# Optimization experiments

Hardware: AMD Instinct MI355X
Metric: run time of the kernel (lower is better)

Reference implementation:

```python
import jax, jax.numpy as jnp
import numpy as np

N = 100000   # nodes
E = 640000   # edges
D = 128      # in_channels
C = 40       # out_channels (classes)


def setup_inputs() -> dict:
    key = jax.random.key(0)
    ks = jax.random.split(key, 6)
    x = jax.random.normal(ks[0], (N, D), jnp.float32)
    edge_index = jax.random.randint(ks[1], (2, E), 0, N)
    edge_weight = jax.random.uniform(ks[2], (E,), jnp.float32)
    # 8 block convs (4 blocks x 2) stacked, + final conv
    Wb = jax.random.normal(ks[3], (8, D, D), jnp.float32) / np.sqrt(D)
    bb = jnp.zeros((8, D), jnp.float32)
    Wf = jax.random.normal(ks[4], (D, C), jnp.float32) / np.sqrt(D)
    bf = jnp.zeros((C,), jnp.float32)
    return dict(x=x, edge_index=edge_index, edge_weight=edge_weight,
                Wb=Wb, bb=bb, Wf=Wf, bf=bf)


def _gcn(x, W, b, src, dst, w):
    """PyG GCNConv (normalize=True) with self-loops already appended to src/dst/w."""
    n = x.shape[0]
    h = x @ W                                   # [N, out]
    deg = jax.ops.segment_sum(w, dst, num_segments=n)
    dinv = jnp.where(deg > 0, jax.lax.rsqrt(deg), 0.0)
    norm = dinv[src] * w * dinv[dst]            # [E+N]
    out = jax.ops.segment_sum(h[src] * norm[:, None], dst, num_segments=n)
    return out + b


def reference(x, edge_index, edge_weight, Wb, bb, Wf, bf):
    n = x.shape[0]
    loop = jnp.arange(n)
    src = jnp.concatenate([edge_index[0], loop])
    dst = jnp.concatenate([edge_index[1], loop])
    w = jnp.concatenate([edge_weight, jnp.ones((n,), x.dtype)])
    # forward only runs blocks 1-4 (blocks 5-7 unused in the original forward)
    for i in range(4):
        identity = x
        x = jax.nn.relu(_gcn(x, Wb[2 * i], bb[2 * i], src, dst, w))
        # dropout: identity in eval mode
        x = jax.nn.relu(_gcn(x, Wb[2 * i + 1], bb[2 * i + 1], src, dst, w))
        # F.normalize: row-wise L2 with eps=1e-12
        x = x / jnp.maximum(jnp.linalg.norm(x, axis=1, keepdims=True), 1e-12)
        x = (x + identity) / 2
    x = _gcn(x, Wf, bf, src, dst, w)
    return jax.nn.log_softmax(x, axis=1)
```

## Files before the change

### kernel.cpp

```cpp
#include <hip/hip_runtime.h>
#include <math.h>

#define NN 100000
#define EE 640000
#define DD 128
#define CC 40

typedef __bf16 bf16x8 __attribute__((ext_vector_type(8)));
typedef float f32x4 __attribute__((ext_vector_type(4)));
typedef unsigned short us8 __attribute__((ext_vector_type(8)));

__device__ inline unsigned short f2b(float f) {
    union { float f; unsigned u; } v; v.f = f;
    unsigned u = v.u;
    return (unsigned short)((u + 0x7FFFu + ((u >> 16) & 1u)) >> 16);
}
__device__ inline float b2f(unsigned short b) {
    union { unsigned u; float f; } v; v.u = ((unsigned)b) << 16;
    return v.f;
}


__global__ __launch_bounds__(256) void k_deg_cnt(const int* __restrict__ dst,
                                                 const float* __restrict__ w,
                                                 float* __restrict__ deg,
                                                 int* __restrict__ cnt) {
    int e = blockIdx.x * 256 + threadIdx.x;
    if (e < EE) {
        int d = dst[e];
        atomicAdd(&deg[d], w[e]);
        atomicAdd(&cnt[d], 1);
    }
}

__global__ __launch_bounds__(256) void k_dinv(float* __restrict__ deg) {
    int i = blockIdx.x * 256 + threadIdx.x;
    if (i < NN) deg[i] = rsqrtf(deg[i] + 1.0f);
}

__global__ __launch_bounds__(256) void k_scan1(const int* __restrict__ cnt,
                                               int* __restrict__ out,
                                               int* __restrict__ partial) {
    __shared__ int lds[256];
    int t = threadIdx.x;
    int base = blockIdx.x * 1024 + t * 4;
    int v[4]; int s = 0;
    #pragma unroll
    for (int j = 0; j < 4; ++j) {
        int idx = base + j;
        v[j] = (idx < NN) ? cnt[idx] : 0;
        s += v[j];
    }
    lds[t] = s;
    __syncthreads();
    for (int off = 1; off < 256; off <<= 1) {
        int x = lds[t];
        int y = (t >= off) ? lds[t - off] : 0;
        __syncthreads();
        lds[t] = x + y;
        __syncthreads();
    }
    int excl = lds[t] - s;
    if (t == 255) partial[blockIdx.x] = lds[255];
    int run = excl;
    #pragma unroll
    for (int j = 0; j < 4; ++j) {
        int idx = base + j;
        if (idx < NN) out[idx] = run;
        run += v[j];
    }
}

__global__ __launch_bounds__(128) void k_scan2(int* __restrict__ partial) {
    __shared__ int lds[128];
    int t = threadIdx.x;
    int v = (t < 98) ? partial[t] : 0;
    lds[t] = v;
    __syncthreads();
    for (int off = 1; off < 128; off <<= 1) {
        int x = lds[t];
        int y = (t >= off) ? lds[t - off] : 0;
        __syncthreads();
        lds[t] = x + y;
        __syncthreads();
    }
    if (t < 98) partial[t] = lds[t] - v;
}

__global__ __launch_bounds__(256) void k_scan3(int* __restrict__ rp,
                                               const int* __restrict__ partial) {
    int i = blockIdx.x * 256 + threadIdx.x;
    if (i < NN) rp[i] += partial[i >> 10];
    if (i == 0) rp[NN] = EE;
}

__global__ __launch_bounds__(256) void k_scatter(const int* __restrict__ src,
                                                 const int* __restrict__ dst,
                                                 const float* __restrict__ w,
                                                 const float* __restrict__ dinv,
                                                 const int* __restrict__ rp,
                                                 int* __restrict__ fill,
                                                 int* __restrict__ col,
                                                 float* __restrict__ val) {
    int e = blockIdx.x * 256 + threadIdx.x;
    if (e < EE) {
        int s = src[e], d = dst[e];
        int p = rp[d] + atomicAdd(&fill[d], 1);
        col[p] = s;
        val[p] = dinv[s] * w[e] * dinv[d];
    }
}


__global__ __launch_bounds__(256) void k_prep_w(const float* __restrict__ Wb,
                                                unsigned short* __restrict__ WT) {
    int idx = blockIdx.x * 256 + threadIdx.x;
    if (idx >= 8 * DD * DD) return;
    int m = idx >> 14;
    int n = (idx >> 7) & 127;
    int k = idx & 127;
    WT[idx] = f2b(Wb[(size_t)m * DD * DD + (size_t)k * DD + n]);
}

__global__ __launch_bounds__(256) void k_prep_wf(const float* __restrict__ Wf,
                                                 unsigned short* __restrict__ WfT) {
    int idx = blockIdx.x * 256 + threadIdx.x;
    if (idx >= 48 * DD) return;
    int n = idx >> 7;
    int k = idx & 127;
    WfT[idx] = (n < CC) ? f2b(Wf[(size_t)k * CC + n]) : 0;
}

__global__ __launch_bounds__(256) void k_x2bf(const float* __restrict__ x,
                                              float* __restrict__ A,
                                              unsigned short* __restrict__ Abf) {
    int idx = blockIdx.x * 256 + threadIdx.x;
    if (idx >= NN * DD / 4) return;
    float4 v = ((const float4*)x)[idx];
    ((float4*)A)[idx] = v;
    ushort4 r;
    r.x = f2b(v.x); r.y = f2b(v.y); r.z = f2b(v.z); r.w = f2b(v.w);
    ((ushort4*)Abf)[idx] = r;
}

__global__ __launch_bounds__(256) void k_mm_mfma(const unsigned short* __restrict__ X,
                                                 const unsigned short* __restrict__ WT,
                                                 unsigned short* __restrict__ H) {
    int wid = threadIdx.x >> 6;
    int lane = threadIdx.x & 63;
    int r0 = blockIdx.x * 64 + wid * 16;
    int sl = lane & 15, g = lane >> 4;
    int arow = r0 + sl;
    if (arow >= NN) arow = NN - 1;

    f32x4 acc[8];
    #pragma unroll
    for (int n = 0; n < 8; ++n) acc[n] = (f32x4){0.f, 0.f, 0.f, 0.f};

    const bf16x8* xrow = (const bf16x8*)(X + (size_t)arow * DD);
    #pragma unroll
    for (int kc = 0; kc < 4; ++kc) {
        bf16x8 a = xrow[kc * 4 + g];
        #pragma unroll
        for (int n = 0; n < 8; ++n) {
            const bf16x8* wrow = (const bf16x8*)(WT + (size_t)(n * 16 + sl) * DD);
            bf16x8 b = wrow[kc * 4 + g];
            acc[n] = __builtin_amdgcn_mfma_f32_16x16x32_bf16(a, b, acc[n], 0, 0, 0);
        }
    }
    #pragma unroll
    for (int n = 0; n < 8; ++n) {
        #pragma unroll
        for (int v = 0; v < 4; ++v) {
            int row = r0 + g * 4 + v;
            if (row < NN) H[(size_t)row * DD + n * 16 + sl] = f2b(acc[n][v]);
        }
    }
}

__global__ __launch_bounds__(256) void k_mm_final(const unsigned short* __restrict__ X,
                                                  const unsigned short* __restrict__ WfT,
                                                  const float* __restrict__ bf_,
                                                  float* __restrict__ C40) {
    int wid = threadIdx.x >> 6;
    int lane = threadIdx.x & 63;
    int r0 = blockIdx.x * 64 + wid * 16;
    int sl = lane & 15, g = lane >> 4;
    int arow = r0 + sl;
    if (arow >= NN) arow = NN - 1;

    f32x4 acc[3];
    #pragma unroll
    for (int n = 0; n < 3; ++n) acc[n] = (f32x4){0.f, 0.f, 0.f, 0.f};

    const bf16x8* xrow = (const bf16x8*)(X + (size_t)arow * DD);
    #pragma unroll
    for (int kc = 0; kc < 4; ++kc) {
        bf16x8 a = xrow[kc * 4 + g];
        #pragma unroll
        for (int n = 0; n < 3; ++n) {
            const bf16x8* wrow = (const bf16x8*)(WfT + (size_t)(n * 16 + sl) * DD);
            bf16x8 b = wrow[kc * 4 + g];
            acc[n] = __builtin_amdgcn_mfma_f32_16x16x32_bf16(a, b, acc[n], 0, 0, 0);
        }
    }
    #pragma unroll
    for (int n = 0; n < 3; ++n) {
        int c = n * 16 + sl;
        #pragma unroll
        for (int v = 0; v < 4; ++v) {
            int row = r0 + g * 4 + v;
            if (row < NN && c < CC) C40[(size_t)row * CC + c] = acc[n][v] + bf_[c];
        }
    }
}


#define AGG_CORE(h_, node_, sl_, a_)                                        \
    {                                                                       \
        float dv = dinv[node_];                                             \
        float dv2 = dv * dv;                                                \
        us8 m_ = ((const us8*)(h_ + (size_t)node_ * DD))[sl_];              \
        _Pragma("unroll")                                                   \
        for (int j = 0; j < 8; ++j) a_[j] = dv2 * b2f(m_[j]);               \
        int e = rp[node_], end = rp[node_ + 1];                             \
        for (; e + 2 <= end; e += 2) {                                      \
            int s0 = col[e], s1 = col[e + 1];                               \
            float v0 = val[e], v1 = val[e + 1];                             \
            us8 q0 = ((const us8*)(h_ + (size_t)s0 * DD))[sl_];             \
            us8 q1 = ((const us8*)(h_ + (size_t)s1 * DD))[sl_];             \
            _Pragma("unroll")                                               \
            for (int j = 0; j < 8; ++j) a_[j] += v0 * b2f(q0[j]) + v1 * b2f(q1[j]); \
        }                                                                   \
        if (e < end) {                                                      \
            int s0 = col[e];                                                \
            float v0 = val[e];                                              \
            us8 q0 = ((const us8*)(h_ + (size_t)s0 * DD))[sl_];             \
            _Pragma("unroll")                                               \
            for (int j = 0; j < 8; ++j) a_[j] += v0 * b2f(q0[j]);           \
        }                                                                   \
    }

__global__ __launch_bounds__(256) void k_agg128(const unsigned short* __restrict__ h,
                                                const float* __restrict__ dinv,
                                                const int* __restrict__ rp,
                                                const int* __restrict__ col,
                                                const float* __restrict__ val,
                                                const float* __restrict__ bias,
                                                unsigned short* __restrict__ outb) {
    int node = blockIdx.x * 16 + (threadIdx.x >> 4);
    int sl = threadIdx.x & 15;
    if (node >= NN) return;
    float a[8];
    AGG_CORE(h, node, sl, a);
    float4 bz0 = ((const float4*)bias)[sl * 2];
    float4 bz1 = ((const float4*)bias)[sl * 2 + 1];
    float bb[8] = {bz0.x, bz0.y, bz0.z, bz0.w, bz1.x, bz1.y, bz1.z, bz1.w};
    us8 r;
    #pragma unroll
    for (int j = 0; j < 8; ++j) r[j] = f2b(fmaxf(a[j] + bb[j], 0.f));
    ((us8*)(outb + (size_t)node * DD))[sl] = r;
}

__global__ __launch_bounds__(256) void k_agg128_nr(const unsigned short* __restrict__ h,
                                                   const float* __restrict__ dinv,
                                                   const int* __restrict__ rp,
                                                   const int* __restrict__ col,
                                                   const float* __restrict__ val,
                                                   const float* __restrict__ bias,
                                                   float* __restrict__ A,
                                                   unsigned short* __restrict__ Abf) {
    int node = blockIdx.x * 16 + (threadIdx.x >> 4);
    int sl = threadIdx.x & 15;
    if (node >= NN) return;
    float a[8];
    AGG_CORE(h, node, sl, a);
    float4 bz0 = ((const float4*)bias)[sl * 2];
    float4 bz1 = ((const float4*)bias)[sl * 2 + 1];
    float bb[8] = {bz0.x, bz0.y, bz0.z, bz0.w, bz1.x, bz1.y, bz1.z, bz1.w};
    float ss = 0.f;
    #pragma unroll
    for (int j = 0; j < 8; ++j) {
        a[j] = fmaxf(a[j] + bb[j], 0.f);
        ss += a[j] * a[j];
    }
    ss += __shfl_xor(ss, 1);
    ss += __shfl_xor(ss, 2);
    ss += __shfl_xor(ss, 4);
    ss += __shfl_xor(ss, 8);
    float sc = 1.0f / fmaxf(sqrtf(ss), 1e-12f);
    float4 a0 = ((const float4*)(A + (size_t)node * DD))[sl * 2];
    float4 a1 = ((const float4*)(A + (size_t)node * DD))[sl * 2 + 1];
    float av[8] = {a0.x, a0.y, a0.z, a0.w, a1.x, a1.y, a1.z, a1.w};
    us8 rb;
    #pragma unroll
    for (int j = 0; j < 8; ++j) {
        av[j] = (a[j] * sc + av[j]) * 0.5f;
        rb[j] = f2b(av[j]);
    }
    float4 o0 = {av[0], av[1], av[2], av[3]};
    float4 o1 = {av[4], av[5], av[6], av[7]};
    ((float4*)(A + (size_t)node * DD))[sl * 2] = o0;
    ((float4*)(A + (size_t)node * DD))[sl * 2 + 1] = o1;
    ((us8*)(Abf + (size_t)node * DD))[sl] = rb;
}

__global__ __launch_bounds__(256) void k_agg_plain(const unsigned short* __restrict__ h,
                                                   const float* __restrict__ dinv,
                                                   const int* __restrict__ rp,
                                                   const int* __restrict__ col,
                                                   const float* __restrict__ val,
                                                   unsigned short* __restrict__ outb) {
    int node = blockIdx.x * 16 + (threadIdx.x >> 4);
    int sl = threadIdx.x & 15;
    if (node >= NN) return;
    float a[8];
    AGG_CORE(h, node, sl, a);
    us8 r;
    #pragma unroll
    for (int j = 0; j < 8; ++j) r[j] = f2b(a[j]);
    ((us8*)(outb + (size_t)node * DD))[sl] = r;
}

__global__ __launch_bounds__(256) void k_logsm(const float* __restrict__ Cb,
                                               float* __restrict__ out) {
    int node = blockIdx.x * 4 + (threadIdx.x >> 6);
    int lane = threadIdx.x & 63;
    if (node >= NN) return;
    float v = (lane < CC) ? Cb[(size_t)node * CC + lane] : -3.0e38f;
    float m = v;
    #pragma unroll
    for (int off = 32; off > 0; off >>= 1) m = fmaxf(m, __shfl_xor(m, off));
    float e = (lane < CC) ? expf(v - m) : 0.f;
    float s = e;
    #pragma unroll
    for (int off = 32; off > 0; off >>= 1) s += __shfl_xor(s, off);
    if (lane < CC) out[(size_t)node * CC + lane] = v - m - logf(s);
}


extern "C" void kernel_launch(void* const* d_in, const int* in_sizes, int n_in,
                              void* d_out, int out_size, void* d_ws, size_t ws_size,
                              hipStream_t stream) {
    const float* x  = (const float*)d_in[0];
    const int*   ei = (const int*)d_in[1];
    const float* ew = (const float*)d_in[2];
    const float* Wb = (const float*)d_in[3];
    const float* bb = (const float*)d_in[4];
    const float* Wf = (const float*)d_in[5];
    const float* bf_ = (const float*)d_in[6];
    const int* src = ei;
    const int* dst = ei + EE;
    float* out = (float*)d_out;

    char* p = (char*)d_ws;
    float*          A    = (float*)p;          p += (size_t)NN * DD * 4;
    unsigned short* Abf  = (unsigned short*)p; p += (size_t)NN * DD * 2;
    unsigned short* Bbf  = (unsigned short*)p; p += (size_t)NN * DD * 2;
    unsigned short* Cbf  = (unsigned short*)p; p += (size_t)NN * DD * 2;
    unsigned short* Gbf  = (unsigned short*)p; p += (size_t)NN * DD * 2;
    float*          C40  = (float*)p;          p += (size_t)NN * CC * 4;
    unsigned short* WT   = (unsigned short*)p; p += (size_t)8 * DD * DD * 2;
    unsigned short* WfT  = (unsigned short*)p; p += (size_t)48 * DD * 2;
    float* dinv = (float*)p; p += (size_t)NN * 4;
    int*   cnt  = (int*)p;   p += (size_t)NN * 4;
    int*   rp   = (int*)p;   p += (size_t)(NN + 1) * 4;
    int*   fill = (int*)p;   p += (size_t)NN * 4;
    int*   col  = (int*)p;   p += (size_t)EE * 4;
    float* val  = (float*)p; p += (size_t)EE * 4;
    int*   partial = (int*)p; p += 128 * 4;

    hipMemsetAsync(dinv, 0, (size_t)NN * 4, stream);
    hipMemsetAsync(cnt,  0, (size_t)NN * 4, stream);
    hipMemsetAsync(fill, 0, (size_t)NN * 4, stream);

    k_deg_cnt<<<(EE + 255) / 256, 256, 0, stream>>>(dst, ew, dinv, cnt);
    k_dinv<<<(NN + 255) / 256, 256, 0, stream>>>(dinv);
    k_scan1<<<98, 256, 0, stream>>>(cnt, rp, partial);
    k_scan2<<<1, 128, 0, stream>>>(partial);
    k_scan3<<<(NN + 255) / 256, 256, 0, stream>>>(rp, partial);
    k_scatter<<<(EE + 255) / 256, 256, 0, stream>>>(src, dst, ew, dinv, rp, fill, col, val);

    k_prep_w<<<(8 * DD * DD + 255) / 256, 256, 0, stream>>>(Wb, WT);
    k_prep_wf<<<(48 * DD + 255) / 256, 256, 0, stream>>>(Wf, WfT);
    k_x2bf<<<(NN * DD / 4 + 255) / 256, 256, 0, stream>>>(x, A, Abf);

    for (int blk = 0; blk < 4; ++blk) {
        k_mm_mfma<<<(NN + 63) / 64, 256, 0, stream>>>(Abf, WT + (size_t)(2 * blk) * DD * DD, Bbf);
        k_agg128<<<(NN + 15) / 16, 256, 0, stream>>>(Bbf, dinv, rp, col, val, bb + (size_t)(2 * blk) * DD, Cbf);
        k_mm_mfma<<<(NN + 63) / 64, 256, 0, stream>>>(Cbf, WT + (size_t)(2 * blk + 1) * DD * DD, Bbf);
        k_agg128_nr<<<(NN + 15) / 16, 256, 0, stream>>>(Bbf, dinv, rp, col, val, bb + (size_t)(2 * blk + 1) * DD, A, Abf);
    }
    k_agg_plain<<<(NN + 15) / 16, 256, 0, stream>>>(Abf, dinv, rp, col, val, Gbf);
    k_mm_final<<<(NN + 63) / 64, 256, 0, stream>>>(Gbf, WfT, bf_, C40);
    k_logsm<<<(NN + 3) / 4, 256, 0, stream>>>(C40, out);
}
```

Before: 793.4 us.

## Pack degree and count atomics, fuse log-softmax into final matmul, unroll aggregation

Packs the fixed-point edge-weight degree and the edge count into a single 64-bit atomic. The returned old count is kept as each edge's slot, which removes the separate fill atomics, the dinv kernel and two memsets. Log-softmax is fused into the final MFMA matmul epilogue, so the C40 intermediate round trip and a kernel launch disappear. The CSR aggregation loop is unrolled from 2 to 4 edges per iteration for more memory-level parallelism. Fixed-point degree accumulation adds a small quantization error in the normalization.

```diff
diff --git a/kernel.cpp b/kernel.cpp
--- a/kernel.cpp
+++ b/kernel.cpp
@@ -5,6 +5,7 @@
 #define EE 640000
 #define DD 128
 #define CC 40
+#define FIXS 4194304.0f
 
 typedef __bf16 bf16x8 __attribute__((ext_vector_type(8)));
 typedef float f32x4 __attribute__((ext_vector_type(4)));
@@ -21,24 +22,22 @@
 }
 
 
-__global__ __launch_bounds__(256) void k_deg_cnt(const int* __restrict__ dst,
-                                                 const float* __restrict__ w,
-                                                 float* __restrict__ deg,
-                                                 int* __restrict__ cnt) {
+__global__ __launch_bounds__(256) void k_edge1(const int* __restrict__ dst,
+                                               const float* __restrict__ w,
+                                               unsigned long long* __restrict__ degcnt,
+                                               int* __restrict__ pos) {
     int e = blockIdx.x * 256 + threadIdx.x;
     if (e < EE) {
         int d = dst[e];
-        atomicAdd(&deg[d], w[e]);
-        atomicAdd(&cnt[d], 1);
-    }
-}
-
-__global__ __launch_bounds__(256) void k_dinv(float* __restrict__ deg) {
-    int i = blockIdx.x * 256 + threadIdx.x;
-    if (i < NN) deg[i] = rsqrtf(deg[i] + 1.0f);
-}
-
-__global__ __launch_bounds__(256) void k_scan1(const int* __restrict__ cnt,
+        unsigned long long pk =
+            ((unsigned long long)(unsigned)(w[e] * FIXS) << 32) | 1ull;
+        unsigned long long old = atomicAdd(&degcnt[d], pk);
+        pos[e] = (int)(old & 0xffffffffull);
+    }
+}
+
+__global__ __launch_bounds__(256) void k_scan1(const unsigned long long* __restrict__ degcnt,
+                                               float* __restrict__ dinv,
                                                int* __restrict__ out,
                                                int* __restrict__ partial) {
     __shared__ int lds[256];
@@ -48,8 +47,11 @@
     #pragma unroll
     for (int j = 0; j < 4; ++j) {
         int idx = base + j;
-        v[j] = (idx < NN) ? cnt[idx] : 0;
+        unsigned long long dc = (idx < NN) ? degcnt[idx] : 0ull;
+        v[j] = (int)(dc & 0xffffffffull);
         s += v[j];
+        if (idx < NN)
+            dinv[idx] = rsqrtf((float)(unsigned)(dc >> 32) * (1.0f / FIXS) + 1.0f);
     }
     lds[t] = s;
     __syncthreads();
@@ -99,13 +101,13 @@
                                                  const float* __restrict__ w,
                                                  const float* __restrict__ dinv,
                                                  const int* __restrict__ rp,
-                                                 int* __restrict__ fill,
+                                                 const int* __restrict__ pos,
                                                  int* __restrict__ col,
                                                  float* __restrict__ val) {
     int e = blockIdx.x * 256 + threadIdx.x;
     if (e < EE) {
         int s = src[e], d = dst[e];
-        int p = rp[d] + atomicAdd(&fill[d], 1);
+        int p = rp[d] + pos[e];
         col[p] = s;
         val[p] = dinv[s] * w[e] * dinv[d];
     }
@@ -181,7 +183,7 @@
 __global__ __launch_bounds__(256) void k_mm_final(const unsigned short* __restrict__ X,
                                                   const unsigned short* __restrict__ WfT,
                                                   const float* __restrict__ bf_,
-                                                  float* __restrict__ C40) {
+                                                  float* __restrict__ out) {
     int wid = threadIdx.x >> 6;
     int lane = threadIdx.x & 63;
     int r0 = blockIdx.x * 64 + wid * 16;
@@ -205,12 +207,32 @@
         }
     }
     #pragma unroll
-    for (int n = 0; n < 3; ++n) {
-        int c = n * 16 + sl;
-        #pragma unroll
-        for (int v = 0; v < 4; ++v) {
-            int row = r0 + g * 4 + v;
-            if (row < NN && c < CC) C40[(size_t)row * CC + c] = acc[n][v] + bf_[c];
+    for (int v = 0; v < 4; ++v) {
+        int row = r0 + g * 4 + v;
+        float vv[3];
+        #pragma unroll
+        for (int n = 0; n < 3; ++n) {
+            int c = n * 16 + sl;
+            vv[n] = (c < CC) ? acc[n][v] + bf_[c] : -3.0e38f;
+        }
+        float m = fmaxf(fmaxf(vv[0], vv[1]), vv[2]);
+        m = fmaxf(m, __shfl_xor(m, 1));
+        m = fmaxf(m, __shfl_xor(m, 2));
+        m = fmaxf(m, __shfl_xor(m, 4));
+        m = fmaxf(m, __shfl_xor(m, 8));
+        float s = 0.f;
+        #pragma unroll
+        for (int n = 0; n < 3; ++n)
+            s += (n * 16 + sl < CC) ? expf(vv[n] - m) : 0.f;
+        s += __shfl_xor(s, 1);
+        s += __shfl_xor(s, 2);
+        s += __shfl_xor(s, 4);
+        s += __shfl_xor(s, 8);
+        float ls = logf(s);
+        #pragma unroll
+        for (int n = 0; n < 3; ++n) {
+            int c = n * 16 + sl;
+            if (row < NN && c < CC) out[(size_t)row * CC + c] = vv[n] - m - ls;
         }
     }
 }
@@ -224,15 +246,19 @@
         _Pragma("unroll")                                                   \
         for (int j = 0; j < 8; ++j) a_[j] = dv2 * b2f(m_[j]);               \
         int e = rp[node_], end = rp[node_ + 1];                             \
-        for (; e + 2 <= end; e += 2) {                                      \
-            int s0 = col[e], s1 = col[e + 1];                               \
-            float v0 = val[e], v1 = val[e + 1];                             \
+        for (; e + 4 <= end; e += 4) {                                      \
+            int s0 = col[e], s1 = col[e + 1], s2 = col[e + 2], s3 = col[e + 3]; \
+            float v0 = val[e], v1 = val[e + 1], v2 = val[e + 2], v3 = val[e + 3]; \
             us8 q0 = ((const us8*)(h_ + (size_t)s0 * DD))[sl_];             \
             us8 q1 = ((const us8*)(h_ + (size_t)s1 * DD))[sl_];             \
+            us8 q2 = ((const us8*)(h_ + (size_t)s2 * DD))[sl_];             \
+            us8 q3 = ((const us8*)(h_ + (size_t)s3 * DD))[sl_];             \
             _Pragma("unroll")                                               \
-            for (int j = 0; j < 8; ++j) a_[j] += v0 * b2f(q0[j]) + v1 * b2f(q1[j]); \
+            for (int j = 0; j < 8; ++j)                                     \
+                a_[j] += (v0 * b2f(q0[j]) + v1 * b2f(q1[j]))                \
+                       + (v2 * b2f(q2[j]) + v3 * b2f(q3[j]));               \
         }                                                                   \
-        if (e < end) {                                                      \
+        for (; e < end; ++e) {                                              \
             int s0 = col[e];                                                \
             float v0 = val[e];                                              \
             us8 q0 = ((const us8*)(h_ + (size_t)s0 * DD))[sl_];             \
@@ -322,22 +348,6 @@
     ((us8*)(outb + (size_t)node * DD))[sl] = r;
 }
 
-__global__ __launch_bounds__(256) void k_logsm(const float* __restrict__ Cb,
-                                               float* __restrict__ out) {
-    int node = blockIdx.x * 4 + (threadIdx.x >> 6);
-    int lane = threadIdx.x & 63;
-    if (node >= NN) return;
-    float v = (lane < CC) ? Cb[(size_t)node * CC + lane] : -3.0e38f;
-    float m = v;
-    #pragma unroll
-    for (int off = 32; off > 0; off >>= 1) m = fmaxf(m, __shfl_xor(m, off));
-    float e = (lane < CC) ? expf(v - m) : 0.f;
-    float s = e;
-    #pragma unroll
-    for (int off = 32; off > 0; off >>= 1) s += __shfl_xor(s, off);
-    if (lane < CC) out[(size_t)node * CC + lane] = v - m - logf(s);
-}
-
 
 extern "C" void kernel_launch(void* const* d_in, const int* in_sizes, int n_in,
                               void* d_out, int out_size, void* d_ws, size_t ws_size,
@@ -354,32 +364,28 @@
     float* out = (float*)d_out;
 
     char* p = (char*)d_ws;
-    float*          A    = (float*)p;          p += (size_t)NN * DD * 4;
-    unsigned short* Abf  = (unsigned short*)p; p += (size_t)NN * DD * 2;
-    unsigned short* Bbf  = (unsigned short*)p; p += (size_t)NN * DD * 2;
-    unsigned short* Cbf  = (unsigned short*)p; p += (size_t)NN * DD * 2;
-    unsigned short* Gbf  = (unsigned short*)p; p += (size_t)NN * DD * 2;
-    float*          C40  = (float*)p;          p += (size_t)NN * CC * 4;
-    unsigned short* WT   = (unsigned short*)p; p += (size_t)8 * DD * DD * 2;
-    unsigned short* WfT  = (unsigned short*)p; p += (size_t)48 * DD * 2;
+    float*              A      = (float*)p;              p += (size_t)NN * DD * 4;
+    unsigned short*     Abf    = (unsigned short*)p;     p += (size_t)NN * DD * 2;
+    unsigned short*     Bbf    = (unsigned short*)p;     p += (size_t)NN * DD * 2;
+    unsigned short*     Cbf    = (unsigned short*)p;     p += (size_t)NN * DD * 2;
+    unsigned short*     Gbf    = (unsigned short*)p;     p += (size_t)NN * DD * 2;
+    unsigned short*     WT     = (unsigned short*)p;     p += (size_t)8 * DD * DD * 2;
+    unsigned short*     WfT    = (unsigned short*)p;     p += (size_t)48 * DD * 2;
+    unsigned long long* degcnt = (unsigned long long*)p; p += (size_t)NN * 8;
     float* dinv = (float*)p; p += (size_t)NN * 4;
-    int*   cnt  = (int*)p;   p += (size_t)NN * 4;
     int*   rp   = (int*)p;   p += (size_t)(NN + 1) * 4;
-    int*   fill = (int*)p;   p += (size_t)NN * 4;
+    int*   pos  = (int*)p;   p += (size_t)EE * 4;
     int*   col  = (int*)p;   p += (size_t)EE * 4;
     float* val  = (float*)p; p += (size_t)EE * 4;
     int*   partial = (int*)p; p += 128 * 4;
 
-    hipMemsetAsync(dinv, 0, (size_t)NN * 4, stream);
-    hipMemsetAsync(cnt,  0, (size_t)NN * 4, stream);
-    hipMemsetAsync(fill, 0, (size_t)NN * 4, stream);
-
-    k_deg_cnt<<<(EE + 255) / 256, 256, 0, stream>>>(dst, ew, dinv, cnt);
-    k_dinv<<<(NN + 255) / 256, 256, 0, stream>>>(dinv);
-    k_scan1<<<98, 256, 0, stream>>>(cnt, rp, partial);
+    hipMemsetAsync(degcnt, 0, (size_t)NN * 8, stream);
+
+    k_edge1<<<(EE + 255) / 256, 256, 0, stream>>>(dst, ew, degcnt, pos);
+    k_scan1<<<98, 256, 0, stream>>>(degcnt, dinv, rp, partial);
     k_scan2<<<1, 128, 0, stream>>>(partial);
     k_scan3<<<(NN + 255) / 256, 256, 0, stream>>>(rp, partial);
-    k_scatter<<<(EE + 255) / 256, 256, 0, stream>>>(src, dst, ew, dinv, rp, fill, col, val);
+    k_scatter<<<(EE + 255) / 256, 256, 0, stream>>>(src, dst, ew, dinv, rp, pos, col, val);
 
     k_prep_w<<<(8 * DD * DD + 255) / 256, 256, 0, stream>>>(Wb, WT);
     k_prep_wf<<<(48 * DD + 255) / 256, 256, 0, stream>>>(Wf, WfT);
@@ -392,6 +398,5 @@
         k_agg128_nr<<<(NN + 15) / 16, 256, 0, stream>>>(Bbf, dinv, rp, col, val, bb + (size_t)(2 * blk + 1) * DD, A, Abf);
     }
     k_agg_plain<<<(NN + 15) / 16, 256, 0, stream>>>(Abf, dinv, rp, col, val, Gbf);
-    k_mm_final<<<(NN + 63) / 64, 256, 0, stream>>>(Gbf, WfT, bf_, C40);
-    k_logsm<<<(NN + 3) / 4, 256, 0, stream>>>(C40, out);
-}
+    k_mm_final<<<(NN + 63) / 64, 256, 0, stream>>>(Gbf, WfT, bf_, out);
+}
```

Result: faster. 725.0 us (-8.6%).
